# Kernel tuning notes

Measured on AMD Instinct MI355X. Metric: run time of the kernel, lower is better.

Reference implementation:

```python
import jax, jax.numpy as jnp
import numpy as np

D_MODEL = 1024
STATE = 16

def setup_inputs() -> dict:
    key = jax.random.key(0)
    ks = jax.random.split(key, 7)
    x = jax.random.normal(ks[0], (4, 4096, D_MODEL), dtype=jnp.float32)
    A_log = jax.random.normal(ks[1], (STATE,), dtype=jnp.float32)
    B = jax.random.normal(ks[2], (STATE, D_MODEL), dtype=jnp.float32) * 0.05
    C = jax.random.normal(ks[3], (D_MODEL, STATE), dtype=jnp.float32) * 0.05
    D = jax.random.normal(ks[4], (D_MODEL,), dtype=jnp.float32)
    W_delta = jax.random.normal(ks[5], (D_MODEL, D_MODEL), dtype=jnp.float32) * 0.02
    b_delta = jax.random.normal(ks[6], (D_MODEL,), dtype=jnp.float32) * 0.02
    return {"x": x, "A_log": A_log, "B": B, "C": C, "D": D,
            "W_delta": W_delta, "b_delta": b_delta}

def reference(x, A_log, B, C, D, W_delta, b_delta):
    # delta: softplus(Linear(x)).mean(-1) -> (b, l)
    delta = jax.nn.softplus(jnp.einsum('bld,ed->ble', x, W_delta) + b_delta).mean(-1)
    A = -jnp.exp(A_log)                         # (n,)
    Bx = jnp.einsum('bld,nd->bln', x, B)        # (b, l, n)
    dA = jnp.exp(delta[..., None] * A)          # (b, l, n)
    dBx = delta[..., None] * Bx                 # (b, l, n)

    def step(h, inp):
        dA_t, dBx_t = inp                       # (b, n) each
        h = dA_t * h + dBx_t
        return h, h

    h0 = jnp.zeros((x.shape[0], A_log.shape[0]), dtype=x.dtype)
    _, hs = jax.lax.scan(step, h0, (jnp.swapaxes(dA, 0, 1), jnp.swapaxes(dBx, 0, 1)))
    hs = jnp.swapaxes(hs, 0, 1)                 # (b, l, n)
    y = jnp.einsum('bln,dn->bld', hs, C) + D * x
    return y
```

## Files before the change

kernel.cpp:

```cpp
#include <hip/hip_runtime.h>
#include <hip/hip_bf16.h>
#include <stdint.h>

#define DM 1024
#define NS 16
#define LSEQ 4096
#define NB 4
#define MTOT (NB*LSEQ)
#define NC 128
#define LC 32

typedef __attribute__((ext_vector_type(8))) short bf16x8;
typedef __attribute__((ext_vector_type(4))) float f32x4;

__device__ __forceinline__ unsigned short f2bf(float f) {
    unsigned int u = __float_as_uint(f);
    unsigned int r = (u + 0x7FFFu + ((u >> 16) & 1u)) >> 16;
    return (unsigned short)r;
}

__device__ __forceinline__ float bf2f(unsigned short u) {
    return __uint_as_float(((unsigned int)u) << 16);
}

__device__ __forceinline__ float softplus_f(float v) {
    return v > 15.f ? v : __logf(1.f + __expf(v));
}

__device__ __forceinline__ void gload_lds16(const void* g, void* l) {
    __builtin_amdgcn_global_load_lds(
        (const __attribute__((address_space(1))) unsigned int*)g,
        (__attribute__((address_space(3))) unsigned int*)l, 16, 0, 0);
}

__global__ __launch_bounds__(256) void pre_kernel(
    const float4* __restrict__ x4, const float4* __restrict__ W4,
    const float4* __restrict__ B4, ushort4* __restrict__ xb4,
    ushort4* __restrict__ wb4, ushort4* __restrict__ bbf4,
    float* __restrict__ delta_raw)
{
    int bid = blockIdx.x, t = threadIdx.x;
    if (bid < 16384) {
        size_t i = (size_t)bid * 256 + t;
        float4 v = x4[i];
        ushort4 o; o.x = f2bf(v.x); o.y = f2bf(v.y); o.z = f2bf(v.z); o.w = f2bf(v.w);
        xb4[i] = o;
    } else if (bid < 17408) {
        int i = (bid - 16384) * 256 + t;
        float4 v = W4[i];
        ushort4 o; o.x = f2bf(v.x); o.y = f2bf(v.y); o.z = f2bf(v.z); o.w = f2bf(v.w);
        wb4[i] = o;
    } else if (bid < 17424) {
        int i = (bid - 17408) * 256 + t;
        float4 v = B4[i];
        ushort4 o; o.x = f2bf(v.x); o.y = f2bf(v.y); o.z = f2bf(v.z); o.w = f2bf(v.w);
        bbf4[i] = o;
    } else {
        int i = (bid - 17424) * 256 + t;
        ((float4*)delta_raw)[i] = (float4){0.f, 0.f, 0.f, 0.f};
    }
}

__global__ __launch_bounds__(512) void gemm_delta(
    const unsigned short* __restrict__ xb, const unsigned short* __restrict__ wb,
    const float* __restrict__ b_delta, float* __restrict__ delta_raw)
{
    __shared__ char lds[131072];
    int bid = blockIdx.x;
    int swz = (bid & 7) * 32 + (bid >> 3);
    int mb = swz >> 2, nb = swz & 3;
    int row0 = mb * 256, e0 = nb * 256;
    int tid = threadIdx.x;
    int lane = tid & 63, w = tid >> 6;
    int wr = w >> 2, wc = w & 3;
    int lm = lane & 15, lk = lane >> 4;

    int colsw = ((lane & 7) * 8) ^ ((lane >> 3) << 3);
    int rsub = lane >> 3;

    const unsigned short* pA[4];
    const unsigned short* pB[4];
    #pragma unroll
    for (int j = 0; j < 4; ++j) {
        int region = w * 4 + j;
        int r0 = region * 8 + rsub;
        pA[j] = xb + (size_t)(row0 + r0) * DM + colsw;
        pB[j] = wb + (size_t)(e0  + r0) * DM + colsw;
    }

    int sterm = (lm & 7) << 4;
    int off0 = (lk * 16) ^ sterm;
    int off1 = (64 + lk * 16) ^ sterm;
    int aBase = (wr * 128 + lm) * 128;
    int bBase = 32768 + (wc * 64 + lm) * 128;

    f32x4 acc[8][4];
    #pragma unroll
    for (int m = 0; m < 8; ++m)
        #pragma unroll
        for (int n = 0; n < 4; ++n)
            acc[m][n] = (f32x4){0.f, 0.f, 0.f, 0.f};

    bf16x8 bq[4][2];

#define STAGE_Q(BUF, Q, KOFF) do { \
    gload_lds16(pA[Q] + (KOFF), lds + (BUF) + ((w * 4 + (Q)) * 1024)); \
    gload_lds16(pB[Q] + (KOFF), lds + (BUF) + 32768 + ((w * 4 + (Q)) * 1024)); \
} while (0)

#define PHASE(CUR, NXT, KOFF, STG, Q) do { \
    if (STG) STAGE_Q(NXT, Q, KOFF); \
    if ((Q) == 0) { \
        if (STG) asm volatile("s_waitcnt vmcnt(2)\n\ts_barrier" ::: "memory"); \
        else     asm volatile("s_waitcnt vmcnt(0)\n\ts_barrier" ::: "memory"); \
        _Pragma("unroll") \
        for (int n = 0; n < 4; ++n) { \
            bq[n][0] = *(const bf16x8*)(lds + (CUR) + bBase + n * 2048 + off0); \
            bq[n][1] = *(const bf16x8*)(lds + (CUR) + bBase + n * 2048 + off1); \
        } \
    } \
    bf16x8 a0 = *(const bf16x8*)(lds + (CUR) + aBase + (2*(Q)) * 2048 + off0); \
    bf16x8 a1 = *(const bf16x8*)(lds + (CUR) + aBase + (2*(Q)) * 2048 + off1); \
    bf16x8 a2 = *(const bf16x8*)(lds + (CUR) + aBase + (2*(Q)+1) * 2048 + off0); \
    bf16x8 a3 = *(const bf16x8*)(lds + (CUR) + aBase + (2*(Q)+1) * 2048 + off1); \
    asm volatile("s_barrier" ::: "memory"); \
    __builtin_amdgcn_s_setprio(1); \
    _Pragma("unroll") \
    for (int n = 0; n < 4; ++n) { \
        acc[2*(Q)][n]   = __builtin_amdgcn_mfma_f32_16x16x32_bf16(a0, bq[n][0], acc[2*(Q)][n], 0, 0, 0); \
        acc[2*(Q)][n]   = __builtin_amdgcn_mfma_f32_16x16x32_bf16(a1, bq[n][1], acc[2*(Q)][n], 0, 0, 0); \
        acc[2*(Q)+1][n] = __builtin_amdgcn_mfma_f32_16x16x32_bf16(a2, bq[n][0], acc[2*(Q)+1][n], 0, 0, 0); \
        acc[2*(Q)+1][n] = __builtin_amdgcn_mfma_f32_16x16x32_bf16(a3, bq[n][1], acc[2*(Q)+1][n], 0, 0, 0); \
    } \
    __builtin_amdgcn_s_setprio(0); \
    asm volatile("s_barrier" ::: "memory"); \
} while (0)

#define KTILE(CUR, NXT, KOFF, STG) do { \
    PHASE(CUR, NXT, KOFF, STG, 0); \
    PHASE(CUR, NXT, KOFF, STG, 1); \
    PHASE(CUR, NXT, KOFF, STG, 2); \
    PHASE(CUR, NXT, KOFF, STG, 3); \
} while (0)

    STAGE_Q(0, 0, 0); STAGE_Q(0, 1, 0); STAGE_Q(0, 2, 0); STAGE_Q(0, 3, 0);
    int koff = 64;
    #pragma unroll 1
    for (int it = 0; it < 7; ++it) {
        KTILE(0,     65536, koff,      true);
        KTILE(65536, 0,     koff + 64, true);
        koff += 128;
    }
    KTILE(0, 65536, 960, true);
    KTILE(65536, 0, 0, false);

#undef KTILE
#undef PHASE
#undef STAGE_Q

    float bd[4];
    #pragma unroll
    for (int n = 0; n < 4; ++n) bd[n] = b_delta[e0 + wc * 64 + n * 16 + lm];
    #pragma unroll
    for (int m = 0; m < 8; ++m) {
        #pragma unroll
        for (int r = 0; r < 4; ++r) {
            float s = 0.f;
            #pragma unroll
            for (int n = 0; n < 4; ++n) s += softplus_f(acc[m][n][r] + bd[n]);
            s += __shfl_xor(s, 1, 16);
            s += __shfl_xor(s, 2, 16);
            s += __shfl_xor(s, 4, 16);
            s += __shfl_xor(s, 8, 16);
            if (lm == 0) {
                int row = row0 + wr * 128 + m * 16 + lk * 4 + r;
                atomicAdd(&delta_raw[row], s);
            }
        }
    }
}

__global__ __launch_bounds__(128) void scan_bx(
    const unsigned short* __restrict__ xb, const unsigned short* __restrict__ bbf,
    const float* __restrict__ delta_raw, const float* __restrict__ A_log,
    float* __restrict__ Bx, float* __restrict__ cP, float* __restrict__ cH)
{
    __shared__ float dl[LC];
    __shared__ float bxl[LC * NS];
    int bid = blockIdx.x;
    int b = bid >> 7, c = bid & 127;
    int t = threadIdx.x;
    int lane = t & 63, w4 = t >> 6;
    size_t base = (size_t)b * LSEQ + c * LC;
    if (t < LC) dl[t] = delta_raw[base + t] * (1.f / 1024.f);

    int lm = lane & 15, lk = lane >> 4;
    const unsigned short* pa = xb + (base + w4 * 16 + lm) * DM + lk * 8;
    const unsigned short* pb = bbf + (size_t)lm * DM + lk * 8;
    f32x4 acc = (f32x4){0.f, 0.f, 0.f, 0.f};
    #pragma unroll 4
    for (int k0 = 0; k0 < DM; k0 += 32) {
        bf16x8 a  = *(const bf16x8*)(pa + k0);
        bf16x8 bb = *(const bf16x8*)(pb + k0);
        acc = __builtin_amdgcn_mfma_f32_16x16x32_bf16(a, bb, acc, 0, 0, 0);
    }
    #pragma unroll
    for (int r = 0; r < 4; ++r) {
        int rl = w4 * 16 + lk * 4 + r;
        bxl[rl * NS + lm] = acc[r];
        Bx[(base + rl) * NS + lm] = acc[r];
    }
    __syncthreads();

    if (t < NS) {
        float a = -__expf(A_log[t]);
        float P = 1.f, h = 0.f;
        #pragma unroll
        for (int s = 0; s < LC; ++s) {
            float dlt = dl[s];
            float dA = __expf(dlt * a);
            h = dA * h + dlt * bxl[s * NS + t];
            P *= dA;
        }
        int idx = (b * NC + c) * NS + t;
        cP[idx] = P; cH[idx] = h;
    }
}

__global__ __launch_bounds__(256) void y_kernel(
    const unsigned short* __restrict__ xb, const float* __restrict__ delta_raw,
    const float* __restrict__ Bx, const float* __restrict__ A_log,
    const float* __restrict__ cP, const float* __restrict__ cH,
    const float* __restrict__ C, const float* __restrict__ Dv, float* __restrict__ y)
{
    __shared__ float dl[LC];
    __shared__ float bxl[LC * NS];
    __shared__ float hsl[LC * NS];
    __shared__ float pbuf[NC * NS];
    __shared__ float hbuf[NC * NS];
    int bid = blockIdx.x;
    int b = bid >> 7, c = bid & 127;
    int l0 = c * LC;
    int t = threadIdx.x;
    size_t base = (size_t)b * LSEQ + l0;
    if (t < LC) dl[t] = delta_raw[base + t] * (1.f / 1024.f);
    if (t < 128) ((float4*)bxl)[t] = ((const float4*)(Bx + base * NS))[t];
    {
        const float4* p4 = (const float4*)(cP + (size_t)b * NC * NS);
        const float4* h4 = (const float4*)(cH + (size_t)b * NC * NS);
        ((float4*)pbuf)[t] = p4[t];         ((float4*)pbuf)[t + 256] = p4[t + 256];
        ((float4*)hbuf)[t] = h4[t];         ((float4*)hbuf)[t + 256] = h4[t + 256];
    }
    __syncthreads();
    if (t < NS) {
        float h = 0.f;
        for (int cc = 0; cc < c; ++cc) {
            int idx = cc * NS + t;
            h = pbuf[idx] * h + hbuf[idx];
        }
        float a = -__expf(A_log[t]);
        #pragma unroll
        for (int s = 0; s < LC; ++s) {
            float dlt = dl[s];
            float dA = __expf(dlt * a);
            h = dA * h + dlt * bxl[s * NS + t];
            hsl[s * NS + t] = h;
        }
    }
    __syncthreads();

    int d0 = t * 4;
    float cr[4][NS];
    #pragma unroll
    for (int dd = 0; dd < 4; ++dd)
        #pragma unroll
        for (int nn = 0; nn < 4; ++nn) {
            float4 c4 = ((const float4*)C)[((d0 + dd) * NS + nn * 4) >> 2];
            cr[dd][nn * 4 + 0] = c4.x; cr[dd][nn * 4 + 1] = c4.y;
            cr[dd][nn * 4 + 2] = c4.z; cr[dd][nn * 4 + 3] = c4.w;
        }
    float4 dv = ((const float4*)Dv)[t];
    const ushort4* xr = (const ushort4*)(xb + base * DM) + t;
    float4* yr = (float4*)(y + base * DM) + t;
    for (int s = 0; s < LC; ++s) {
        float hv[NS];
        #pragma unroll
        for (int n = 0; n < NS; ++n) hv[n] = hsl[s * NS + n];
        ushort4 xv4 = xr[s * 256];
        float4 o;
        o.x = dv.x * bf2f(xv4.x); o.y = dv.y * bf2f(xv4.y);
        o.z = dv.z * bf2f(xv4.z); o.w = dv.w * bf2f(xv4.w);
        #pragma unroll
        for (int n = 0; n < NS; ++n) {
            o.x += hv[n] * cr[0][n];
            o.y += hv[n] * cr[1][n];
            o.z += hv[n] * cr[2][n];
            o.w += hv[n] * cr[3][n];
        }
        yr[s * 256] = o;
    }
}

extern "C" void kernel_launch(void* const* d_in, const int* in_sizes, int n_in,
                              void* d_out, int out_size, void* d_ws, size_t ws_size,
                              hipStream_t stream)
{
    const float* x     = (const float*)d_in[0];
    const float* A_log = (const float*)d_in[1];
    const float* B     = (const float*)d_in[2];
    const float* C     = (const float*)d_in[3];
    const float* Dv    = (const float*)d_in[4];
    const float* Wd    = (const float*)d_in[5];
    const float* bd    = (const float*)d_in[6];
    float* y = (float*)d_out;

    char* ws = (char*)d_ws;
    unsigned short* xb = (unsigned short*)ws;
    unsigned short* wb = (unsigned short*)(ws + 33554432);
    float* delta_raw   = (float*)(ws + 35651584);
    float* Bx          = (float*)(ws + 35717120);
    float* cP          = (float*)(ws + 36765696);
    float* cH          = (float*)(ws + 36798464);
    unsigned short* bbf= (unsigned short*)(ws + 36831232);

    pre_kernel<<<17440, 256, 0, stream>>>((const float4*)x, (const float4*)Wd,
                                          (const float4*)B, (ushort4*)xb,
                                          (ushort4*)wb, (ushort4*)bbf, delta_raw);
    gemm_delta<<<256, 512, 0, stream>>>(xb, wb, bd, delta_raw);
    scan_bx<<<NB * NC, 128, 0, stream>>>(xb, bbf, delta_raw, A_log, Bx, cP, cH);
    y_kernel<<<NB * NC, 256, 0, stream>>>(xb, delta_raw, Bx, A_log, cP, cH, C, Dv, y);
}
```

Measured before the change: 92.39 us.

## Fuse delta GEMM, chunk scan and output into one cooperative kernel

Merges the delta GEMM, the chunked scan with Bx projection, and the y-output kernel into a single cooperative kernel of 256 blocks that separates stages with grid-wide syncs. Each block now handles two chunks in the scan and output stages, and Bx stays in LDS instead of making a round trip through global memory. This removes two kernel launches and the Bx buffer traffic. In exchange it adds grid-sync overhead and gives the later stages only 256 blocks instead of 512, which may reduce parallelism in the memory-bound y stage.

```diff
diff --git a/kernel.cpp b/kernel.cpp
--- a/kernel.cpp
+++ b/kernel.cpp
@@ -1,6 +1,9 @@
 #include <hip/hip_runtime.h>
 #include <hip/hip_bf16.h>
+#include <hip/hip_cooperative_groups.h>
 #include <stdint.h>
+
+namespace cg = cooperative_groups;
 
 #define DM 1024
 #define NS 16
@@ -61,47 +64,53 @@
     }
 }
 
-__global__ __launch_bounds__(512) void gemm_delta(
+__global__ __launch_bounds__(512) void fused_main(
     const unsigned short* __restrict__ xb, const unsigned short* __restrict__ wb,
-    const float* __restrict__ b_delta, float* __restrict__ delta_raw)
+    const unsigned short* __restrict__ bbf, const float* __restrict__ b_delta,
+    float* __restrict__ delta_raw, const float* __restrict__ A_log,
+    float* __restrict__ cP, float* __restrict__ cH,
+    const float* __restrict__ C, const float* __restrict__ Dv, float* __restrict__ y)
 {
     __shared__ char lds[131072];
-    int bid = blockIdx.x;
-    int swz = (bid & 7) * 32 + (bid >> 3);
-    int mb = swz >> 2, nb = swz & 3;
-    int row0 = mb * 256, e0 = nb * 256;
-    int tid = threadIdx.x;
-    int lane = tid & 63, w = tid >> 6;
-    int wr = w >> 2, wc = w & 3;
-    int lm = lane & 15, lk = lane >> 4;
-
-    int colsw = ((lane & 7) * 8) ^ ((lane >> 3) << 3);
-    int rsub = lane >> 3;
-
-    const unsigned short* pA[4];
-    const unsigned short* pB[4];
-    #pragma unroll
-    for (int j = 0; j < 4; ++j) {
-        int region = w * 4 + j;
-        int r0 = region * 8 + rsub;
-        pA[j] = xb + (size_t)(row0 + r0) * DM + colsw;
-        pB[j] = wb + (size_t)(e0  + r0) * DM + colsw;
-    }
-
-    int sterm = (lm & 7) << 4;
-    int off0 = (lk * 16) ^ sterm;
-    int off1 = (64 + lk * 16) ^ sterm;
-    int aBase = (wr * 128 + lm) * 128;
-    int bBase = 32768 + (wc * 64 + lm) * 128;
-
-    f32x4 acc[8][4];
-    #pragma unroll
-    for (int m = 0; m < 8; ++m)
-        #pragma unroll
-        for (int n = 0; n < 4; ++n)
-            acc[m][n] = (f32x4){0.f, 0.f, 0.f, 0.f};
-
-    bf16x8 bq[4][2];
+    cg::grid_group grid = cg::this_grid();
+
+    {
+        int bid = blockIdx.x;
+        int swz = (bid & 7) * 32 + (bid >> 3);
+        int mb = swz >> 2, nb = swz & 3;
+        int row0 = mb * 256, e0 = nb * 256;
+        int tid = threadIdx.x;
+        int lane = tid & 63, w = tid >> 6;
+        int wr = w >> 2, wc = w & 3;
+        int lm = lane & 15, lk = lane >> 4;
+
+        int colsw = ((lane & 7) * 8) ^ ((lane >> 3) << 3);
+        int rsub = lane >> 3;
+
+        const unsigned short* pA[4];
+        const unsigned short* pB[4];
+        #pragma unroll
+        for (int j = 0; j < 4; ++j) {
+            int region = w * 4 + j;
+            int r0 = region * 8 + rsub;
+            pA[j] = xb + (size_t)(row0 + r0) * DM + colsw;
+            pB[j] = wb + (size_t)(e0  + r0) * DM + colsw;
+        }
+
+        int sterm = (lm & 7) << 4;
+        int off0 = (lk * 16) ^ sterm;
+        int off1 = (64 + lk * 16) ^ sterm;
+        int aBase = (wr * 128 + lm) * 128;
+        int bBase = 32768 + (wc * 64 + lm) * 128;
+
+        f32x4 acc[8][4];
+        #pragma unroll
+        for (int m = 0; m < 8; ++m)
+            #pragma unroll
+            for (int n = 0; n < 4; ++n)
+                acc[m][n] = (f32x4){0.f, 0.f, 0.f, 0.f};
+
+        bf16x8 bq[4][2];
 
 #define STAGE_Q(BUF, Q, KOFF) do { \
     gload_lds16(pA[Q] + (KOFF), lds + (BUF) + ((w * 4 + (Q)) * 1024)); \
@@ -143,161 +152,158 @@
     PHASE(CUR, NXT, KOFF, STG, 3); \
 } while (0)
 
-    STAGE_Q(0, 0, 0); STAGE_Q(0, 1, 0); STAGE_Q(0, 2, 0); STAGE_Q(0, 3, 0);
-    int koff = 64;
-    #pragma unroll 1
-    for (int it = 0; it < 7; ++it) {
-        KTILE(0,     65536, koff,      true);
-        KTILE(65536, 0,     koff + 64, true);
-        koff += 128;
-    }
-    KTILE(0, 65536, 960, true);
-    KTILE(65536, 0, 0, false);
+        STAGE_Q(0, 0, 0); STAGE_Q(0, 1, 0); STAGE_Q(0, 2, 0); STAGE_Q(0, 3, 0);
+        int koff = 64;
+        #pragma unroll 1
+        for (int it = 0; it < 7; ++it) {
+            KTILE(0,     65536, koff,      true);
+            KTILE(65536, 0,     koff + 64, true);
+            koff += 128;
+        }
+        KTILE(0, 65536, 960, true);
+        KTILE(65536, 0, 0, false);
 
 #undef KTILE
 #undef PHASE
 #undef STAGE_Q
 
-    float bd[4];
-    #pragma unroll
-    for (int n = 0; n < 4; ++n) bd[n] = b_delta[e0 + wc * 64 + n * 16 + lm];
-    #pragma unroll
-    for (int m = 0; m < 8; ++m) {
-        #pragma unroll
-        for (int r = 0; r < 4; ++r) {
-            float s = 0.f;
-            #pragma unroll
-            for (int n = 0; n < 4; ++n) s += softplus_f(acc[m][n][r] + bd[n]);
-            s += __shfl_xor(s, 1, 16);
-            s += __shfl_xor(s, 2, 16);
-            s += __shfl_xor(s, 4, 16);
-            s += __shfl_xor(s, 8, 16);
-            if (lm == 0) {
-                int row = row0 + wr * 128 + m * 16 + lk * 4 + r;
-                atomicAdd(&delta_raw[row], s);
+        float bd[4];
+        #pragma unroll
+        for (int n = 0; n < 4; ++n) bd[n] = b_delta[e0 + wc * 64 + n * 16 + lm];
+        #pragma unroll
+        for (int m = 0; m < 8; ++m) {
+            #pragma unroll
+            for (int r = 0; r < 4; ++r) {
+                float s = 0.f;
+                #pragma unroll
+                for (int n = 0; n < 4; ++n) s += softplus_f(acc[m][n][r] + bd[n]);
+                s += __shfl_xor(s, 1, 16);
+                s += __shfl_xor(s, 2, 16);
+                s += __shfl_xor(s, 4, 16);
+                s += __shfl_xor(s, 8, 16);
+                if (lm == 0) {
+                    int row = row0 + wr * 128 + m * 16 + lk * 4 + r;
+                    atomicAdd(&delta_raw[row], s);
+                }
             }
         }
     }
-}
-
-__global__ __launch_bounds__(128) void scan_bx(
-    const unsigned short* __restrict__ xb, const unsigned short* __restrict__ bbf,
-    const float* __restrict__ delta_raw, const float* __restrict__ A_log,
-    float* __restrict__ Bx, float* __restrict__ cP, float* __restrict__ cH)
-{
-    __shared__ float dl[LC];
-    __shared__ float bxl[LC * NS];
-    int bid = blockIdx.x;
-    int b = bid >> 7, c = bid & 127;
-    int t = threadIdx.x;
-    int lane = t & 63, w4 = t >> 6;
-    size_t base = (size_t)b * LSEQ + c * LC;
-    if (t < LC) dl[t] = delta_raw[base + t] * (1.f / 1024.f);
-
-    int lm = lane & 15, lk = lane >> 4;
-    const unsigned short* pa = xb + (base + w4 * 16 + lm) * DM + lk * 8;
-    const unsigned short* pb = bbf + (size_t)lm * DM + lk * 8;
-    f32x4 acc = (f32x4){0.f, 0.f, 0.f, 0.f};
-    #pragma unroll 4
-    for (int k0 = 0; k0 < DM; k0 += 32) {
-        bf16x8 a  = *(const bf16x8*)(pa + k0);
-        bf16x8 bb = *(const bf16x8*)(pb + k0);
-        acc = __builtin_amdgcn_mfma_f32_16x16x32_bf16(a, bb, acc, 0, 0, 0);
+
+    grid.sync();
+
+    float* dl   = (float*)(lds);
+    float* bxl  = (float*)(lds + 1024);
+    float* hsl  = (float*)(lds + 8192);
+    float* pbuf = (float*)(lds + 16384);
+    float* hbuf = (float*)(lds + 32768);
+
+    int bid = blockIdx.x, t = threadIdx.x;
+    int gc0 = bid * 2;
+    int b = gc0 >> 7, c0 = gc0 & 127;
+    size_t base0 = (size_t)b * LSEQ + c0 * LC;
+    size_t base1 = base0 + LC;
+
+    {
+        if (t < 32)                      dl[t]            = delta_raw[base0 + t] * (1.f / 1024.f);
+        else if (t >= 256 && t < 288)    dl[32 + t - 256] = delta_raw[base1 + t - 256] * (1.f / 1024.f);
+
+        int w = t >> 6;
+        if (w < 4) {
+            int lane = t & 63, lm = lane & 15, lk = lane >> 4;
+            int ch = w >> 1;
+            size_t rbase = (ch ? base1 : base0) + (size_t)(w & 1) * 16;
+            const unsigned short* pa = xb + (rbase + lm) * DM + lk * 8;
+            const unsigned short* pb = bbf + (size_t)lm * DM + lk * 8;
+            f32x4 acc = (f32x4){0.f, 0.f, 0.f, 0.f};
+            #pragma unroll 4
+            for (int k0 = 0; k0 < DM; k0 += 32) {
+                bf16x8 a  = *(const bf16x8*)(pa + k0);
+                bf16x8 bb = *(const bf16x8*)(pb + k0);
+                acc = __builtin_amdgcn_mfma_f32_16x16x32_bf16(a, bb, acc, 0, 0, 0);
+            }
+            #pragma unroll
+            for (int r = 0; r < 4; ++r) {
+                int rl = (w & 1) * 16 + lk * 4 + r;
+                bxl[ch * 512 + rl * NS + lm] = acc[r];
+            }
+        }
+        __syncthreads();
+
+        if ((t < 16) || (t >= 256 && t < 272)) {
+            int ch = t >> 8, n = t & 15;
+            float a = -__expf(A_log[n]);
+            float P = 1.f, h = 0.f;
+            #pragma unroll
+            for (int s = 0; s < LC; ++s) {
+                float dlt = dl[ch * 32 + s];
+                float dA = __expf(dlt * a);
+                h = dA * h + dlt * bxl[ch * 512 + s * NS + n];
+                P *= dA;
+            }
+            int idx = (b * NC + c0 + ch) * NS + n;
+            cP[idx] = P; cH[idx] = h;
+        }
     }
-    #pragma unroll
-    for (int r = 0; r < 4; ++r) {
-        int rl = w4 * 16 + lk * 4 + r;
-        bxl[rl * NS + lm] = acc[r];
-        Bx[(base + rl) * NS + lm] = acc[r];
-    }
-    __syncthreads();
-
-    if (t < NS) {
-        float a = -__expf(A_log[t]);
-        float P = 1.f, h = 0.f;
-        #pragma unroll
-        for (int s = 0; s < LC; ++s) {
-            float dlt = dl[s];
-            float dA = __expf(dlt * a);
-            h = dA * h + dlt * bxl[s * NS + t];
-            P *= dA;
-        }
-        int idx = (b * NC + c) * NS + t;
-        cP[idx] = P; cH[idx] = h;
-    }
-}
-
-__global__ __launch_bounds__(256) void y_kernel(
-    const unsigned short* __restrict__ xb, const float* __restrict__ delta_raw,
-    const float* __restrict__ Bx, const float* __restrict__ A_log,
-    const float* __restrict__ cP, const float* __restrict__ cH,
-    const float* __restrict__ C, const float* __restrict__ Dv, float* __restrict__ y)
-{
-    __shared__ float dl[LC];
-    __shared__ float bxl[LC * NS];
-    __shared__ float hsl[LC * NS];
-    __shared__ float pbuf[NC * NS];
-    __shared__ float hbuf[NC * NS];
-    int bid = blockIdx.x;
-    int b = bid >> 7, c = bid & 127;
-    int l0 = c * LC;
-    int t = threadIdx.x;
-    size_t base = (size_t)b * LSEQ + l0;
-    if (t < LC) dl[t] = delta_raw[base + t] * (1.f / 1024.f);
-    if (t < 128) ((float4*)bxl)[t] = ((const float4*)(Bx + base * NS))[t];
+
+    grid.sync();
+
     {
         const float4* p4 = (const float4*)(cP + (size_t)b * NC * NS);
         const float4* h4 = (const float4*)(cH + (size_t)b * NC * NS);
-        ((float4*)pbuf)[t] = p4[t];         ((float4*)pbuf)[t + 256] = p4[t + 256];
-        ((float4*)hbuf)[t] = h4[t];         ((float4*)hbuf)[t + 256] = h4[t + 256];
-    }
-    __syncthreads();
-    if (t < NS) {
-        float h = 0.f;
-        for (int cc = 0; cc < c; ++cc) {
-            int idx = cc * NS + t;
-            h = pbuf[idx] * h + hbuf[idx];
-        }
-        float a = -__expf(A_log[t]);
-        #pragma unroll
+        ((float4*)pbuf)[t] = p4[t];
+        ((float4*)hbuf)[t] = h4[t];
+        __syncthreads();
+
+        if ((t < 16) || (t >= 256 && t < 272)) {
+            int ch = t >> 8, n = t & 15;
+            int c = c0 + ch;
+            float h = 0.f;
+            for (int cc = 0; cc < c; ++cc)
+                h = pbuf[cc * NS + n] * h + hbuf[cc * NS + n];
+            float a = -__expf(A_log[n]);
+            #pragma unroll
+            for (int s = 0; s < LC; ++s) {
+                float dlt = dl[ch * 32 + s];
+                float dA = __expf(dlt * a);
+                h = dA * h + dlt * bxl[ch * 512 + s * NS + n];
+                hsl[ch * 512 + s * NS + n] = h;
+            }
+        }
+        __syncthreads();
+
+        int tl = t & 255, ch = t >> 8;
+        size_t base = (size_t)b * LSEQ + (size_t)(c0 + ch) * LC;
+        int d0 = tl * 4;
+        float cr[4][NS];
+        #pragma unroll
+        for (int dd = 0; dd < 4; ++dd)
+            #pragma unroll
+            for (int nn = 0; nn < 4; ++nn) {
+                float4 c4 = ((const float4*)C)[((d0 + dd) * NS + nn * 4) >> 2];
+                cr[dd][nn * 4 + 0] = c4.x; cr[dd][nn * 4 + 1] = c4.y;
+                cr[dd][nn * 4 + 2] = c4.z; cr[dd][nn * 4 + 3] = c4.w;
+            }
+        float4 dv = ((const float4*)Dv)[tl];
+        const ushort4* xr = (const ushort4*)(xb + base * DM) + tl;
+        float4* yr = (float4*)(y + base * DM) + tl;
+        const float* hs = hsl + ch * 512;
         for (int s = 0; s < LC; ++s) {
-            float dlt = dl[s];
-            float dA = __expf(dlt * a);
-            h = dA * h + dlt * bxl[s * NS + t];
-            hsl[s * NS + t] = h;
-        }
-    }
-    __syncthreads();
-
-    int d0 = t * 4;
-    float cr[4][NS];
-    #pragma unroll
-    for (int dd = 0; dd < 4; ++dd)
-        #pragma unroll
-        for (int nn = 0; nn < 4; ++nn) {
-            float4 c4 = ((const float4*)C)[((d0 + dd) * NS + nn * 4) >> 2];
-            cr[dd][nn * 4 + 0] = c4.x; cr[dd][nn * 4 + 1] = c4.y;
-            cr[dd][nn * 4 + 2] = c4.z; cr[dd][nn * 4 + 3] = c4.w;
-        }
-    float4 dv = ((const float4*)Dv)[t];
-    const ushort4* xr = (const ushort4*)(xb + base * DM) + t;
-    float4* yr = (float4*)(y + base * DM) + t;
-    for (int s = 0; s < LC; ++s) {
-        float hv[NS];
-        #pragma unroll
-        for (int n = 0; n < NS; ++n) hv[n] = hsl[s * NS + n];
-        ushort4 xv4 = xr[s * 256];
-        float4 o;
-        o.x = dv.x * bf2f(xv4.x); o.y = dv.y * bf2f(xv4.y);
-        o.z = dv.z * bf2f(xv4.z); o.w = dv.w * bf2f(xv4.w);
-        #pragma unroll
-        for (int n = 0; n < NS; ++n) {
-            o.x += hv[n] * cr[0][n];
-            o.y += hv[n] * cr[1][n];
-            o.z += hv[n] * cr[2][n];
-            o.w += hv[n] * cr[3][n];
-        }
-        yr[s * 256] = o;
+            float hv[NS];
+            #pragma unroll
+            for (int n = 0; n < NS; ++n) hv[n] = hs[s * NS + n];
+            ushort4 xv4 = xr[s * 256];
+            float4 o;
+            o.x = dv.x * bf2f(xv4.x); o.y = dv.y * bf2f(xv4.y);
+            o.z = dv.z * bf2f(xv4.z); o.w = dv.w * bf2f(xv4.w);
+            #pragma unroll
+            for (int n = 0; n < NS; ++n) {
+                o.x += hv[n] * cr[0][n];
+                o.y += hv[n] * cr[1][n];
+                o.z += hv[n] * cr[2][n];
+                o.w += hv[n] * cr[3][n];
+            }
+            yr[s * 256] = o;
+        }
     }
 }
 
@@ -318,7 +324,6 @@
     unsigned short* xb = (unsigned short*)ws;
     unsigned short* wb = (unsigned short*)(ws + 33554432);
     float* delta_raw   = (float*)(ws + 35651584);
-    float* Bx          = (float*)(ws + 35717120);
     float* cP          = (float*)(ws + 36765696);
     float* cH          = (float*)(ws + 36798464);
     unsigned short* bbf= (unsigned short*)(ws + 36831232);
@@ -326,7 +331,8 @@
     pre_kernel<<<17440, 256, 0, stream>>>((const float4*)x, (const float4*)Wd,
                                           (const float4*)B, (ushort4*)xb,
                                           (ushort4*)wb, (ushort4*)bbf, delta_raw);
-    gemm_delta<<<256, 512, 0, stream>>>(xb, wb, bd, delta_raw);
-    scan_bx<<<NB * NC, 128, 0, stream>>>(xb, bbf, delta_raw, A_log, Bx, cP, cH);
-    y_kernel<<<NB * NC, 256, 0, stream>>>(xb, delta_raw, Bx, A_log, cP, cH, C, Dv, y);
-}
+
+    void* kargs[] = {(void*)&xb, (void*)&wb, (void*)&bbf, (void*)&bd, (void*)&delta_raw,
+                     (void*)&A_log, (void*)&cP, (void*)&cH, (void*)&C, (void*)&Dv, (void*)&y};
+    hipLaunchCooperativeKernel((void*)fused_main, dim3(256), dim3(512), kargs, 0, stream);
+}
```

Result: slower. 143.7 us (+55.5%).
